# Kernel optimization log

Hardware: AMD Instinct MI355X
Metric: run time of the kernel (lower is better)

Reference implementation:

```python
import jax, jax.numpy as jnp
import numpy as np

D = 1024        # hidden_size
H = 16          # num_heads
HD = D // H     # head_dim = 64
K = 4           # conv kernel size
I = int(D * 2.7)  # ffn intermediate = 2764
B, T = 2, 2048
EPS = 1e-6
GATE_BIAS = 4.0


def setup_inputs() -> dict:
    key = jax.random.key(0)
    ks = jax.random.split(key, 16)
    s = D ** -0.5
    return {
        "x": jax.random.normal(ks[0], (B, T, D), jnp.float32),
        "norm1_w": jnp.ones((D,), jnp.float32),
        "norm2_w": jnp.ones((D,), jnp.float32),
        "conv_w": jax.random.normal(ks[1], (D, K), jnp.float32) * 0.2,
        "conv_b": jnp.zeros((D,), jnp.float32),
        "wq": jax.random.normal(ks[2], (D, D), jnp.float32) * s,
        "wk": jax.random.normal(ks[3], (D, D), jnp.float32) * s,
        "wv": jax.random.normal(ks[4], (D, D), jnp.float32) * s,
        "wb": jax.random.normal(ks[5], (D, H), jnp.float32) * s,
        "wa": jax.random.normal(ks[6], (D, H), jnp.float32) * s,
        "wo": jax.random.normal(ks[7], (D, D), jnp.float32) * s,
        "wg": jax.random.normal(ks[8], (D, I), jnp.float32) * s,
        "wu": jax.random.normal(ks[9], (D, I), jnp.float32) * s,
        "wd": jax.random.normal(ks[10], (I, D), jnp.float32) * (I ** -0.5),
    }


def _rmsnorm(x, w):
    return x * jax.lax.rsqrt(jnp.mean(x * x, axis=-1, keepdims=True) + EPS) * w


def _causal_depthwise_conv(x, conv_w, conv_b):
    # x: [B,T,D]; depthwise causal conv, kernel K, then SiLU
    xt = jnp.transpose(x, (0, 2, 1))  # [B,D,T]
    y = jax.lax.conv_general_dilated(
        xt, conv_w[:, None, :],  # [D,1,K]
        window_strides=(1,), padding=[(K - 1, 0)],
        feature_group_count=D,
        dimension_numbers=("NCH", "OIH", "NCH"))
    y = jnp.transpose(y, (0, 2, 1)) + conv_b  # [B,T,D]
    return jax.nn.silu(y)


def _l2norm(x):
    return x * jax.lax.rsqrt(jnp.sum(x * x, axis=-1, keepdims=True) + EPS)


def _gated_delta_rule(xc, wq, wk, wv, wb, wa):
    b, t = xc.shape[0], xc.shape[1]
    q = _l2norm((xc @ wq).reshape(b, t, H, HD))
    k = _l2norm((xc @ wk).reshape(b, t, H, HD))
    v = (xc @ wv).reshape(b, t, H, HD)
    beta = jax.nn.sigmoid(xc @ wb)              # [B,T,H]
    alpha = jax.nn.sigmoid(xc @ wa + GATE_BIAS)  # [B,T,H] decay gate

    # time-major for scan
    qt = jnp.moveaxis(q, 1, 0)
    kt = jnp.moveaxis(k, 1, 0)
    vt = jnp.moveaxis(v, 1, 0)
    bt = jnp.moveaxis(beta, 1, 0)
    at = jnp.moveaxis(alpha, 1, 0)

    S0 = jnp.zeros((b, H, HD, HD), xc.dtype)  # [B,H,dk,dv]

    def step(S, inp):
        q_, k_, v_, b_, a_ = inp
        S = a_[..., None, None] * S
        pred = jnp.einsum("bhkv,bhk->bhv", S, k_)
        S = S + k_[..., :, None] * (b_[..., None] * (v_ - pred))[..., None, :]
        o = jnp.einsum("bhkv,bhk->bhv", S, q_)
        return S, o

    _, o = jax.lax.scan(step, S0, (qt, kt, vt, bt, at))  # [T,B,H,HD]
    return jnp.moveaxis(o, 1, 0).reshape(b, t, D)


def reference(x, norm1_w, norm2_w, conv_w, conv_b, wq, wk, wv, wb, wa, wo,
              wg, wu, wd):
    residual = x
    xn = _rmsnorm(x, norm1_w)
    xc = _causal_depthwise_conv(xn, conv_w, conv_b)
    mixer_out = _gated_delta_rule(xc, wq, wk, wv, wb, wa) @ wo
    h = residual + mixer_out
    hn = _rmsnorm(h, norm2_w)
    ffn = (jax.nn.silu(hn @ wg) * (hn @ wu)) @ wd
    return h + ffn
```

## Files before the change

kernel.cpp:

```cpp
#include <hip/hip_runtime.h>
#include <math.h>

#define D_ 1024
#define H_ 16
#define HD_ 64
#define KW_ 4
#define I_ 2764
#define IP_ 2816
#define NQKV_ 3328
#define NGU_ 5632
#define B_ 2
#define T_ 2048
#define BT_ (B_*T_)
#define ND_ (BT_*D_)
#define NH_ (BT_*H_)
#define NCH_ 32
#define NG_ (32*NCH_)
#define EPS_ 1e-6f
#define GATE_BIAS_ 4.0f

typedef __attribute__((ext_vector_type(8))) short bf16x8;
typedef __attribute__((ext_vector_type(4))) float f32x4;

#define MFMA_(a,b,c) __builtin_amdgcn_mfma_f32_16x16x32_bf16(a, b, c, 0, 0, 0)
#define GLDS_(src, dst) __builtin_amdgcn_global_load_lds( \
    (const __attribute__((address_space(1))) void*)(src), \
    (__attribute__((address_space(3))) void*)(dst), 16, 0, 0)

__device__ float f_sc1[BT_];
__device__ float f_be[NH_];
__device__ float f_al[NH_];
__device__ float f_h[ND_];
__device__ float g_rs[NG_ * 256];
__device__ float g_BmT[(size_t)NG_*4096];
__device__ unsigned short g_Gqk[(size_t)NG_*4096];
__device__ unsigned short g_Y[(size_t)NG_*4096];
__device__ unsigned short g_ZT[(size_t)NG_*4096];
__device__ unsigned short g_A[(size_t)NG_*4096];
__device__ unsigned short g_S[(size_t)NG_*4096];
__device__ unsigned short b_q[ND_];
__device__ unsigned short b_k[ND_];
__device__ unsigned short b_v[ND_];
__device__ unsigned short b_xc[ND_];
__device__ unsigned short b_o[ND_];
__device__ unsigned short b_hn[ND_];
__device__ unsigned short b_f[(size_t)BT_*IP_];
__device__ unsigned short b_wqkvT[(size_t)NQKV_*D_];
__device__ unsigned short b_woT[D_*D_];
__device__ unsigned short b_wguT[(size_t)NGU_*D_];
__device__ unsigned short b_wdT[(size_t)D_*IP_];

__device__ __forceinline__ unsigned short f2b(float x) {
  union { float f; unsigned u; } a; a.f = x;
  unsigned r = a.u + 0x7fff + ((a.u >> 16) & 1);
  return (unsigned short)(r >> 16);
}
__device__ __forceinline__ float b2f(unsigned short s) {
  union { unsigned u; float f; } a; a.u = ((unsigned)s) << 16; return a.f;
}

__device__ __forceinline__ const unsigned short* bsel(int id) {
  switch (id) {
    case 0: return b_xc;  case 1: return b_o;    case 2: return b_hn;
    case 3: return b_f;   case 4: return b_wqkvT; case 5: return b_woT;
    case 6: return b_wguT; default: return b_wdT;
  }
}
__device__ __forceinline__ unsigned short* bselw(int id) {
  return (unsigned short*)bsel(id);
}

__global__ __launch_bounds__(256) void rmssc_k(const float* __restrict__ x) {
  int row = blockIdx.x;
  int tid = threadIdx.x;
  float4 v = ((const float4*)(x + (size_t)row * D_))[tid];
  float ss = v.x*v.x + v.y*v.y + v.z*v.z + v.w*v.w;
  #pragma unroll
  for (int o = 32; o > 0; o >>= 1) ss += __shfl_down(ss, o);
  __shared__ float sred[4];
  if ((tid & 63) == 0) sred[tid >> 6] = ss;
  __syncthreads();
  if (tid == 0)
    f_sc1[row] = rsqrtf((sred[0]+sred[1]+sred[2]+sred[3]) / (float)D_ + EPS_);
}

__global__ __launch_bounds__(256) void rms2_k(const float* __restrict__ w) {
  int row = blockIdx.x;
  const float* xr = f_h + (size_t)row * D_;
  int tid = threadIdx.x;
  float4 v = ((const float4*)xr)[tid];
  float ss = v.x*v.x + v.y*v.y + v.z*v.z + v.w*v.w;
  #pragma unroll
  for (int o = 32; o > 0; o >>= 1) ss += __shfl_down(ss, o);
  __shared__ float sred[4];
  __shared__ float sscale;
  if ((tid & 63) == 0) sred[tid >> 6] = ss;
  __syncthreads();
  if (tid == 0)
    sscale = rsqrtf((sred[0]+sred[1]+sred[2]+sred[3]) / (float)D_ + EPS_);
  __syncthreads();
  float s = sscale;
  float4 wv = ((const float4*)w)[tid];
  unsigned short* orow = b_hn + (size_t)row * D_ + tid * 4;
  orow[0] = f2b(v.x*s*wv.x); orow[1] = f2b(v.y*s*wv.y);
  orow[2] = f2b(v.z*s*wv.z); orow[3] = f2b(v.w*s*wv.w);
}

__global__ __launch_bounds__(256) void conv2_k(const float* __restrict__ x,
                                               const float* __restrict__ cw,
                                               const float* __restrict__ cb,
                                               const float* __restrict__ n1w) {
  int idx = blockIdx.x * 256 + threadIdx.x;
  int d = idx & (D_ - 1);
  int bt = idx >> 10;
  int t = bt & (T_ - 1);
  float wd = n1w[d];
  float acc = cb[d];
  #pragma unroll
  for (int j = 0; j < KW_; j++) {
    int tt = t - (KW_ - 1) + j;
    if (tt >= 0) {
      int off = j - (KW_ - 1);
      acc += x[(size_t)idx + (size_t)off * D_] * f_sc1[bt + off] * wd * cw[d * KW_ + j];
    }
  }
  float s = acc / (1.f + expf(-acc));
  b_xc[idx] = f2b(s);
}

__global__ __launch_bounds__(256) void castTqkv_k(const float* __restrict__ wq,
                                                  const float* __restrict__ wk,
                                                  const float* __restrict__ wv,
                                                  const float* __restrict__ wb,
                                                  const float* __restrict__ wa) {
  __shared__ float s[64][65];
  int n0 = blockIdx.x * 64, k0 = blockIdx.y * 64;
  int tx = threadIdx.x & 63, ty = threadIdx.x >> 6;
  int nn = n0 + tx;
  const float* src = nullptr; int col = 0, ld = 1024;
  if (nn < 1024)      { src = wq; col = nn; }
  else if (nn < 2048) { src = wk; col = nn - 1024; }
  else if (nn < 3072) { src = wv; col = nn - 2048; }
  else if (nn < 3088) { src = wb; col = nn - 3072; ld = 16; }
  else if (nn < 3104) { src = wa; col = nn - 3088; ld = 16; }
  #pragma unroll
  for (int j = ty; j < 64; j += 4)
    s[j][tx] = src ? src[(size_t)(k0 + j) * ld + col] : 0.f;
  __syncthreads();
  #pragma unroll
  for (int j = ty; j < 64; j += 4)
    b_wqkvT[(size_t)(n0 + j) * D_ + k0 + tx] = f2b(s[tx][j]);
}

__global__ __launch_bounds__(256) void castTgu_k(const float* __restrict__ wg,
                                                 const float* __restrict__ wu) {
  __shared__ float s[64][65];
  int n0 = blockIdx.x * 64, k0 = blockIdx.y * 64;
  int tx = threadIdx.x & 63, ty = threadIdx.x >> 6;
  int nn = n0 + tx;
  int inner = nn & 31;
  int col = (nn >> 5) * 16 + (inner & 15);
  const float* src = (inner < 16) ? wg : wu;
  bool ok = (col < I_);
  #pragma unroll
  for (int j = ty; j < 64; j += 4)
    s[j][tx] = ok ? src[(size_t)(k0 + j) * I_ + col] : 0.f;
  __syncthreads();
  #pragma unroll
  for (int j = ty; j < 64; j += 4)
    b_wguT[(size_t)(n0 + j) * D_ + k0 + tx] = f2b(s[tx][j]);
}

__global__ __launch_bounds__(256) void castT_k(const float* __restrict__ W,
                                               int K, int N, int outid, int Kp) {
  __shared__ float s[64][65];
  unsigned short* out = bselw(outid);
  int k0 = blockIdx.y * 64, n0 = blockIdx.x * 64;
  int tx = threadIdx.x & 63, ty = threadIdx.x >> 6;
  #pragma unroll
  for (int j = ty; j < 64; j += 4) {
    int kk = k0 + j, nn = n0 + tx;
    s[j][tx] = (kk < K && nn < N) ? W[(size_t)kk * N + nn] : 0.f;
  }
  __syncthreads();
  #pragma unroll
  for (int j = ty; j < 64; j += 4)
    out[(size_t)(n0 + j) * Kp + k0 + tx] = f2b(s[tx][j]);
}

__global__ __launch_bounds__(512) void gemm256(int aid, int bid, int Kp, int mode) {
  __shared__ __align__(16) unsigned short Al[2][256 * 64];
  __shared__ __align__(16) unsigned short Bl[2][256 * 64];
  const unsigned short* A = bsel(aid);
  const unsigned short* Bt = bsel(bid);
  int tid = threadIdx.x;
  int nbx = gridDim.x;
  int nwg = nbx * gridDim.y;
  int lid = blockIdx.y * nbx + blockIdx.x;
  int cpx = nwg >> 3;
  int swzb = (lid & 7) * cpx + (lid >> 3);
  int m0 = (swzb / nbx) * 256, n0 = (swzb % nbx) * 256;
  int w = tid >> 6, lane = tid & 63;
  int wm = (w >> 2) * 128, wn = (w & 3) * 64;
  const int l15 = lane & 15, lg = lane >> 4;
  int srow = tid >> 3;
  int scol = ((tid & 7) ^ (srow & 7)) * 8;
  int ldsw = w * 512;
  const unsigned short* Arow = A + (size_t)m0 * Kp;
  const unsigned short* Brow = Bt + (size_t)n0 * Kp;
  int swz0 = ((0 + lg) ^ (l15 & 7)) * 8;
  int swz1 = ((4 + lg) ^ (l15 & 7)) * 8;
  f32x4 acc[8][4] = {};
  const int nt = Kp >> 6;
  #pragma unroll
  for (int i = 0; i < 4; i++) {
    GLDS_(Arow + (size_t)(i * 64 + srow) * Kp + scol, Al[0] + i * 4096 + ldsw);
    GLDS_(Brow + (size_t)(i * 64 + srow) * Kp + scol, Bl[0] + i * 4096 + ldsw);
  }
  asm volatile("s_waitcnt vmcnt(0)" ::: "memory");
  __builtin_amdgcn_s_barrier();
  int cur = 0;
  for (int t = 0; t < nt; t++) {
    if (t + 1 < nt) {
      int k0 = (t + 1) << 6;
      #pragma unroll
      for (int i = 0; i < 4; i++) {
        GLDS_(Arow + (size_t)(i * 64 + srow) * Kp + k0 + scol, Al[cur ^ 1] + i * 4096 + ldsw);
        GLDS_(Brow + (size_t)(i * 64 + srow) * Kp + k0 + scol, Bl[cur ^ 1] + i * 4096 + ldsw);
      }
    }
    __builtin_amdgcn_s_setprio(1);
    {
      bf16x8 af[8], bf[4];
      #pragma unroll
      for (int i = 0; i < 8; i++)
        af[i] = *(const bf16x8*)&Al[cur][(wm + i * 16 + l15) * 64 + swz0];
      #pragma unroll
      for (int j = 0; j < 4; j++)
        bf[j] = *(const bf16x8*)&Bl[cur][(wn + j * 16 + l15) * 64 + swz0];
      #pragma unroll
      for (int i = 0; i < 8; i++)
        #pragma unroll
        for (int j = 0; j < 4; j++)
          acc[i][j] = MFMA_(af[i], bf[j], acc[i][j]);
      #pragma unroll
      for (int i = 0; i < 8; i++)
        af[i] = *(const bf16x8*)&Al[cur][(wm + i * 16 + l15) * 64 + swz1];
      #pragma unroll
      for (int j = 0; j < 4; j++)
        bf[j] = *(const bf16x8*)&Bl[cur][(wn + j * 16 + l15) * 64 + swz1];
      #pragma unroll
      for (int i = 0; i < 8; i++)
        #pragma unroll
        for (int j = 0; j < 4; j++)
          acc[i][j] = MFMA_(af[i], bf[j], acc[i][j]);
    }
    __builtin_amdgcn_s_setprio(0);
    __builtin_amdgcn_sched_barrier(0);
    asm volatile("s_waitcnt vmcnt(0)" ::: "memory");
    __builtin_amdgcn_s_barrier();
    __builtin_amdgcn_sched_barrier(0);
    cur ^= 1;
  }
  int C0 = n0 + wn;
  if (mode == 0) {
    if (C0 < 2048) {
      unsigned short* dst = (C0 < 1024) ? b_q : b_k;
      int cbase = C0 & 1023;
      #pragma unroll
      for (int i = 0; i < 8; i++) {
        int r0i = m0 + wm + i * 16 + lg * 4;
        #pragma unroll
        for (int r = 0; r < 4; r++) {
          float ss = acc[i][0][r]*acc[i][0][r] + acc[i][1][r]*acc[i][1][r]
                   + acc[i][2][r]*acc[i][2][r] + acc[i][3][r]*acc[i][3][r];
          ss += __shfl_xor(ss, 1); ss += __shfl_xor(ss, 2);
          ss += __shfl_xor(ss, 4); ss += __shfl_xor(ss, 8);
          float sc = rsqrtf(ss + EPS_);
          #pragma unroll
          for (int j = 0; j < 4; j++)
            dst[(size_t)(r0i + r) * D_ + cbase + j * 16 + l15] = f2b(acc[i][j][r] * sc);
        }
      }
    } else if (C0 < 3072) {
      int cbase = C0 & 1023;
      #pragma unroll
      for (int i = 0; i < 8; i++) {
        int r0i = m0 + wm + i * 16 + lg * 4;
        #pragma unroll
        for (int j = 0; j < 4; j++)
          #pragma unroll
          for (int r = 0; r < 4; r++)
            b_v[(size_t)(r0i + r) * D_ + cbase + j * 16 + l15] = f2b(acc[i][j][r]);
      }
    } else if (C0 == 3072) {
      #pragma unroll
      for (int i = 0; i < 8; i++) {
        int r0i = m0 + wm + i * 16 + lg * 4;
        #pragma unroll
        for (int r = 0; r < 4; r++) {
          float vb = acc[i][0][r];
          f_be[(size_t)(r0i + r) * H_ + l15] = 1.f / (1.f + expf(-vb));
          float va = acc[i][1][r] + GATE_BIAS_;
          f_al[(size_t)(r0i + r) * H_ + l15] = 1.f / (1.f + expf(-va));
        }
      }
    }
  } else {
    #pragma unroll
    for (int i = 0; i < 8; i++) {
      int r0i = m0 + wm + i * 16 + lg * 4;
      #pragma unroll
      for (int jp = 0; jp < 2; jp++) {
        int j = jp * 2;
        int Lbase = ((C0 + j * 16) >> 5) * 16;
        #pragma unroll
        for (int r = 0; r < 4; r++) {
          float g = acc[i][j][r], u = acc[i][j + 1][r];
          float sg = g / (1.f + expf(-g));
          b_f[(size_t)(r0i + r) * IP_ + Lbase + l15] = f2b(sg * u);
        }
      }
    }
  }
}

__global__ __launch_bounds__(256) void gemm_bf16(int aid, int bid, int Kp, int mode,
                                                 const float* __restrict__ ext,
                                                 float* __restrict__ eout) {
  __shared__ __align__(16) unsigned short Al[3][128 * 32];
  __shared__ __align__(16) unsigned short Bl[3][128 * 32];
  const unsigned short* A = bsel(aid);
  const unsigned short* Bt = bsel(bid);
  int tid = threadIdx.x;
  int nbx = gridDim.x;
  int nwg = nbx * gridDim.y;
  int lid = blockIdx.y * nbx + blockIdx.x;
  int cpx = nwg >> 3;
  int swzb = (lid & 7) * cpx + (lid >> 3);
  int m0 = (swzb / nbx) * 128, n0 = (swzb % nbx) * 128;
  int wave = tid >> 6, lane = tid & 63;
  int wm = (wave >> 1) * 64, wn = (wave & 1) * 64;
  int lrow = tid >> 2;
  int lcol = ((tid & 3) ^ ((lrow >> 1) & 3)) * 8;
  f32x4 acc[4][4] = {};
  const int l15 = lane & 15, lg = lane >> 4;
  const int sw = (lg ^ ((l15 >> 1) & 3)) * 8;
  const int nt = Kp >> 5;
  const unsigned short* Arow = A + (size_t)m0 * Kp;
  const unsigned short* Brow = Bt + (size_t)n0 * Kp;
  {
    GLDS_(Arow + (size_t)lrow * Kp + lcol,        Al[0] + wave * 512);
    GLDS_(Arow + (size_t)(64 + lrow) * Kp + lcol, Al[0] + 2048 + wave * 512);
    GLDS_(Brow + (size_t)lrow * Kp + lcol,        Bl[0] + wave * 512);
    GLDS_(Brow + (size_t)(64 + lrow) * Kp + lcol, Bl[0] + 2048 + wave * 512);
    GLDS_(Arow + (size_t)lrow * Kp + 32 + lcol,        Al[1] + wave * 512);
    GLDS_(Arow + (size_t)(64 + lrow) * Kp + 32 + lcol, Al[1] + 2048 + wave * 512);
    GLDS_(Brow + (size_t)lrow * Kp + 32 + lcol,        Bl[1] + wave * 512);
    GLDS_(Brow + (size_t)(64 + lrow) * Kp + 32 + lcol, Bl[1] + 2048 + wave * 512);
  }
  int c0i = 0, c1i = 1, c2i = 2;
  for (int t = 0; t < nt; t++) {
    if (t + 2 < nt) {
      int k0 = (t + 2) << 5;
      GLDS_(Arow + (size_t)lrow * Kp + k0 + lcol,        Al[c2i] + wave * 512);
      GLDS_(Arow + (size_t)(64 + lrow) * Kp + k0 + lcol, Al[c2i] + 2048 + wave * 512);
      GLDS_(Brow + (size_t)lrow * Kp + k0 + lcol,        Bl[c2i] + wave * 512);
      GLDS_(Brow + (size_t)(64 + lrow) * Kp + k0 + lcol, Bl[c2i] + 2048 + wave * 512);
      asm volatile("s_waitcnt vmcnt(8)" ::: "memory");
    } else if (t + 1 < nt) {
      asm volatile("s_waitcnt vmcnt(4)" ::: "memory");
    } else {
      asm volatile("s_waitcnt vmcnt(0)" ::: "memory");
    }
    __builtin_amdgcn_sched_barrier(0);
    __builtin_amdgcn_s_barrier();
    __builtin_amdgcn_sched_barrier(0);
    bf16x8 af[4], bf[4];
    #pragma unroll
    for (int i = 0; i < 4; i++)
      af[i] = *(const bf16x8*)&Al[c0i][(wm + i * 16 + l15) * 32 + sw];
    #pragma unroll
    for (int j = 0; j < 4; j++)
      bf[j] = *(const bf16x8*)&Bl[c0i][(wn + j * 16 + l15) * 32 + sw];
    #pragma unroll
    for (int i = 0; i < 4; i++)
      #pragma unroll
      for (int j = 0; j < 4; j++)
        acc[i][j] = MFMA_(af[i], bf[j], acc[i][j]);
    __builtin_amdgcn_sched_barrier(0);
    __builtin_amdgcn_s_barrier();
    __builtin_amdgcn_sched_barrier(0);
    int tmp = c0i; c0i = c1i; c1i = c2i; c2i = tmp;
  }
  int C0 = n0 + wn;
  if (mode == 2) {
    #pragma unroll
    for (int i = 0; i < 4; i++) {
      int r0i = m0 + wm + i * 16 + lg * 4;
      #pragma unroll
      for (int j = 0; j < 4; j++)
        #pragma unroll
        for (int r = 0; r < 4; r++) {
          size_t off = (size_t)(r0i + r) * D_ + C0 + j * 16 + l15;
          f_h[off] = ext[off] + acc[i][j][r];
        }
    }
  } else {
    #pragma unroll
    for (int i = 0; i < 4; i++) {
      int r0i = m0 + wm + i * 16 + lg * 4;
      #pragma unroll
      for (int j = 0; j < 4; j++)
        #pragma unroll
        for (int r = 0; r < 4; r++) {
          size_t off = (size_t)(r0i + r) * D_ + C0 + j * 16 + l15;
          eout[off] = f_h[off] + acc[i][j][r];
        }
    }
  }
}


__global__ __launch_bounds__(256) void prep_k() {
  __shared__ __align__(16) char sm[40448];
  unsigned short* sKT = (unsigned short*)sm;
  unsigned short* sVT = (unsigned short*)(sm + 10240);
  unsigned short* sAb = (unsigned short*)(sm + 20480);
  unsigned short* sYT = (unsigned short*)(sm + 20480);
  unsigned short* sXb = (unsigned short*)(sm + 29696);
  float* sL  = (float*)(sm + 38912);
  float* sB  = (float*)(sm + 39168);
  float* sS2 = (float*)(sm + 39424);
  float* sDec= (float*)(sm + 39680);
  float* sGC = (float*)(sm + 39936);

  int gid = blockIdx.x;
  int ch = gid & 31, bh = gid >> 5;
  int b = bh >> 4, h = bh & 15;
  int c0 = ch * 64, hb = h * HD_;
  int rowb = b * T_ + c0;
  int tid = threadIdx.x;
  int w = tid >> 6, lane = tid & 63, l15 = lane & 15, lg = lane >> 4;
  size_t g4 = (size_t)gid * 4096;

  if (tid < 64) {
    size_t rb = ((size_t)(rowb + tid)) * H_ + h;
    float la = log2f(f_al[rb]);
    #pragma unroll
    for (int m = 1; m < 64; m <<= 1) {
      float o = __shfl_up(la, m);
      if (tid >= m) la += o;
    }
    float L63 = __shfl(la, 63);
    float bt = f_be[rb];
    float g = exp2f(la);
    sL[tid] = la; sB[tid] = bt; sS2[tid] = bt * g;
    sDec[tid] = exp2f(L63 - la);
    if (tid == 63) sGC[0] = g;
    g_rs[(size_t)gid*256 + tid*4 + 0] = bt;
    g_rs[(size_t)gid*256 + tid*4 + 1] = bt * g;
    g_rs[(size_t)gid*256 + tid*4 + 2] = g;
  }
  __syncthreads();

  {
    int tp = tid >> 3, q8 = tid & 7;
    int t0 = 2 * tp, t1 = 2 * tp + 1;
    const bf16x8 k0 = *(const bf16x8*)(b_k + (size_t)(rowb + t0) * D_ + hb + q8 * 8);
    const bf16x8 k1 = *(const bf16x8*)(b_k + (size_t)(rowb + t1) * D_ + hb + q8 * 8);
    const bf16x8 v0 = *(const bf16x8*)(b_v + (size_t)(rowb + t0) * D_ + hb + q8 * 8);
    const bf16x8 v1 = *(const bf16x8*)(b_v + (size_t)(rowb + t1) * D_ + hb + q8 * 8);
    float s0 = sB[t0], s1v = sB[t1];
    unsigned* KT32 = (unsigned*)sKT;
    unsigned* VT32 = (unsigned*)sVT;
    #pragma unroll
    for (int i = 0; i < 8; i++) {
      int k = q8 * 8 + i;
      KT32[k*40 + tp] = (unsigned)(unsigned short)k0[i] |
                        ((unsigned)(unsigned short)k1[i] << 16);
      unsigned lo = f2b(b2f((unsigned short)v0[i]) * s0);
      unsigned hi = f2b(b2f((unsigned short)v1[i]) * s1v);
      VT32[k*40 + tp] = lo | (hi << 16);
    }
  }
  {
    bf16x8 bK[2], aK[4][2], aQ[4][2];
    #pragma unroll
    for (int k2 = 0; k2 < 2; k2++) {
      bK[k2] = *(const bf16x8*)&b_k[(size_t)(rowb + w*16 + l15)*D_ + hb + k2*32 + lg*8];
      #pragma unroll
      for (int ti = 0; ti < 4; ti++) {
        aK[ti][k2] = *(const bf16x8*)&b_k[(size_t)(rowb + ti*16 + l15)*D_ + hb + k2*32 + lg*8];
        aQ[ti][k2] = *(const bf16x8*)&b_q[(size_t)(rowb + ti*16 + l15)*D_ + hb + k2*32 + lg*8];
      }
    }
    f32x4 ck[4] = {}, cq[4] = {};
    #pragma unroll
    for (int k2 = 0; k2 < 2; k2++)
      #pragma unroll
      for (int ti = 0; ti < 4; ti++) {
        ck[ti] = MFMA_(aK[ti][k2], bK[k2], ck[ti]);
        cq[ti] = MFMA_(aQ[ti][k2], bK[k2], cq[ti]);
      }
    int j = w*16 + l15;
    float Lj = sL[j];
    #pragma unroll
    for (int ti = 0; ti < 4; ti++)
      #pragma unroll
      for (int r = 0; r < 4; r++) {
        int t = ti*16 + lg*4 + r;
        float ratio = exp2f(sL[t] - Lj);
        sAb[t*72 + j] = f2b((j < t) ? sB[t] * ratio * ck[ti][r] : 0.f);
        g_Gqk[g4 + t*64 + j] = f2b((j <= t) ? ratio * cq[ti][r] : 0.f);
      }
  }
  __syncthreads();
  {
    int c = (w << 4) + (lane >> 2);
    int p = lane & 3;
    int rb16 = p << 4;
    float xr[16];
    #pragma unroll
    for (int j = 0; j < 16; j++) xr[j] = 0.f;
    #pragma unroll
    for (int q = 0; q < 16; q++) {
      int r0 = 4 * q;
      const unsigned short* abr = sAb + r0 * 72 + rb16;
      bf16x8 A0a = *(const bf16x8*)(abr);
      bf16x8 A0b = *(const bf16x8*)(abr + 8);
      bf16x8 A1a = *(const bf16x8*)(abr + 72);
      bf16x8 A1b = *(const bf16x8*)(abr + 80);
      bf16x8 A2a = *(const bf16x8*)(abr + 144);
      bf16x8 A2b = *(const bf16x8*)(abr + 152);
      bf16x8 A3a = *(const bf16x8*)(abr + 216);
      bf16x8 A3b = *(const bf16x8*)(abr + 224);
      float s0 = 0.f, s1 = 0.f, s2 = 0.f, s3 = 0.f;
      #pragma unroll
      for (int j = 0; j < 8; j++) {
        float xv = xr[j], xw = xr[8 + j];
        s0 = fmaf(b2f((unsigned short)A0a[j]), xv, s0);
        s1 = fmaf(b2f((unsigned short)A1a[j]), xv, s1);
        s2 = fmaf(b2f((unsigned short)A2a[j]), xv, s2);
        s3 = fmaf(b2f((unsigned short)A3a[j]), xv, s3);
        s0 = fmaf(b2f((unsigned short)A0b[j]), xw, s0);
        s1 = fmaf(b2f((unsigned short)A1b[j]), xw, s1);
        s2 = fmaf(b2f((unsigned short)A2b[j]), xw, s2);
        s3 = fmaf(b2f((unsigned short)A3b[j]), xw, s3);
      }
      s0 += __shfl_xor(s0, 1); s0 += __shfl_xor(s0, 2);
      s1 += __shfl_xor(s1, 1); s1 += __shfl_xor(s1, 2);
      s2 += __shfl_xor(s2, 1); s2 += __shfl_xor(s2, 2);
      s3 += __shfl_xor(s3, 1); s3 += __shfl_xor(s3, 2);
      float a10 = b2f(sAb[(r0+1)*72 + r0]);
      float a20 = b2f(sAb[(r0+2)*72 + r0]);
      float a21 = b2f(sAb[(r0+2)*72 + r0+1]);
      float a30 = b2f(sAb[(r0+3)*72 + r0]);
      float a31 = b2f(sAb[(r0+3)*72 + r0+1]);
      float a32 = b2f(sAb[(r0+3)*72 + r0+2]);
      float x0 = ((r0+0) == c ? 1.f : 0.f) - s0;
      float x1 = ((r0+1) == c ? 1.f : 0.f) - s1 - a10*x0;
      float x2 = ((r0+2) == c ? 1.f : 0.f) - s2 - a20*x0 - a21*x1;
      float x3 = ((r0+3) == c ? 1.f : 0.f) - s3 - a30*x0 - a31*x1 - a32*x2;
      if (p == (q >> 2)) {
        int ji = 4 * (q & 3);
        xr[ji+0] = x0; xr[ji+1] = x1; xr[ji+2] = x2; xr[ji+3] = x3;
      }
    }
    #pragma unroll
    for (int j = 0; j < 16; j++)
      sXb[(rb16 + j)*72 + c] = f2b(xr[j]);
  }
  __syncthreads();
  int m0 = w * 16;
  f32x4 cyT[4], cz[4];
  {
    bf16x8 aKT[2];
    aKT[0] = *(const bf16x8*)&sKT[(m0 + l15)*80 + lg*8];
    aKT[1] = *(const bf16x8*)&sKT[(m0 + l15)*80 + 32 + lg*8];
    #pragma unroll
    for (int n = 0; n < 4; n++) {
      cyT[n] = f32x4{0.f, 0.f, 0.f, 0.f};
      #pragma unroll
      for (int k2 = 0; k2 < 2; k2++) {
        bf16x8 bb;
        #pragma unroll
        for (int i = 0; i < 8; i++) {
          int tp = k2*32 + lg*8 + i;
          bb[i] = (short)f2b(b2f(sXb[(n*16 + l15)*72 + tp]) * sS2[tp]);
        }
        cyT[n] = MFMA_(aKT[k2], bb, cyT[n]);
      }
    }
    bf16x8 aT2[2];
    #pragma unroll
    for (int k2 = 0; k2 < 2; k2++)
      #pragma unroll
      for (int i = 0; i < 8; i++) {
        int tp = k2*32 + lg*8 + i;
        aT2[k2][i] = (short)f2b(b2f(sXb[(m0 + l15)*72 + tp]) * sS2[tp]);
      }
    #pragma unroll
    for (int n = 0; n < 4; n++) {
      f32x4 c = {};
      #pragma unroll
      for (int k2 = 0; k2 < 2; k2++) {
        bf16x8 bKT = *(const bf16x8*)&sKT[(n*16 + l15)*80 + k2*32 + lg*8];
        c = MFMA_(aT2[k2], bKT, c);
      }
      #pragma unroll
      for (int r = 0; r < 4; r++)
        g_Y[g4 + (m0 + lg*4 + r)*64 + n*16 + l15] = f2b(c[r]);
    }
    bf16x8 aV[2];
    aV[0] = *(const bf16x8*)&sVT[(m0 + l15)*80 + lg*8];
    aV[1] = *(const bf16x8*)&sVT[(m0 + l15)*80 + 32 + lg*8];
    #pragma unroll
    for (int n = 0; n < 4; n++) {
      cz[n] = f32x4{0.f, 0.f, 0.f, 0.f};
      #pragma unroll
      for (int k2 = 0; k2 < 2; k2++) {
        bf16x8 bT = *(const bf16x8*)&sXb[(n*16 + l15)*72 + k2*32 + lg*8];
        cz[n] = MFMA_(aV[k2], bT, cz[n]);
      }
      #pragma unroll
      for (int r = 0; r < 4; r++)
        g_ZT[g4 + (m0 + lg*4 + r)*64 + n*16 + l15] = f2b(cz[n][r]);
    }
  }
  __syncthreads();
  #pragma unroll
  for (int n = 0; n < 4; n++)
    #pragma unroll
    for (int r = 0; r < 4; r++) {
      sYT[(m0 + lg*4 + r)*72 + n*16 + l15] = f2b(cyT[n][r]);
      sVT[(m0 + lg*4 + r)*80 + n*16 + l15] = f2b(cz[n][r]);
    }
  {
    int xx = tid >> 2, q = tid & 3;
    bf16x8 v0 = *(const bf16x8*)&sKT[xx*80 + q*16];
    bf16x8 v1 = *(const bf16x8*)&sKT[xx*80 + q*16 + 8];
    bf16x8 d0, d1;
    #pragma unroll
    for (int i = 0; i < 8; i++) {
      d0[i] = (short)f2b(b2f((unsigned short)v0[i]) * sDec[q*16 + i]);
      d1[i] = (short)f2b(b2f((unsigned short)v1[i]) * sDec[q*16 + 8 + i]);
    }
    *(bf16x8*)&sKT[xx*80 + q*16] = d0;
    *(bf16x8*)&sKT[xx*80 + q*16 + 8] = d1;
  }
  __syncthreads();
  {
    float gC = sGC[0];
    bf16x8 aKd[2];
    aKd[0] = *(const bf16x8*)&sKT[(m0 + l15)*80 + lg*8];
    aKd[1] = *(const bf16x8*)&sKT[(m0 + l15)*80 + 32 + lg*8];
    #pragma unroll
    for (int n = 0; n < 4; n++) {
      f32x4 c = {};
      #pragma unroll
      for (int k2 = 0; k2 < 2; k2++) {
        bf16x8 bY = *(const bf16x8*)&sYT[(n*16 + l15)*72 + k2*32 + lg*8];
        c = MFMA_(aKd[k2], bY, c);
      }
      #pragma unroll
      for (int r = 0; r < 4; r++) {
        int row = m0 + lg*4 + r, col = n*16 + l15;
        g_A[g4 + row*64 + col] = f2b(((row == col) ? gC : 0.f) - c[r]);
      }
    }
    #pragma unroll
    for (int n = 0; n < 4; n++) {
      f32x4 c = {};
      #pragma unroll
      for (int k2 = 0; k2 < 2; k2++) {
        bf16x8 bZ = *(const bf16x8*)&sVT[(n*16 + l15)*80 + k2*32 + lg*8];
        c = MFMA_(aKd[k2], bZ, c);
      }
      *(f32x4*)&g_BmT[g4 + (size_t)(n*16 + l15)*64 + m0 + lg*4] = c;
    }
  }
}

__global__ __launch_bounds__(256) void seq_k() {
  __shared__ __align__(16) unsigned short sST[4][16*80];
  int bh = blockIdx.x;
  int tid = threadIdx.x, w = tid >> 6, lane = tid & 63;
  int l15 = lane & 15, lg = lane >> 4;
  unsigned short* st = sST[w];
  for (int i = lane; i < 16*80; i += 64) st[i] = 0;
  f32x4 cerr[4] = {};
  bf16x8 aA[4][2];
  f32x4 cini[4];
  size_t g40 = (size_t)(bh * 32) * 4096;
  #pragma unroll
  for (int m = 0; m < 4; m++) {
    aA[m][0] = *(const bf16x8*)&g_A[g40 + (m*16 + l15)*64 + lg*8];
    aA[m][1] = *(const bf16x8*)&g_A[g40 + (m*16 + l15)*64 + 32 + lg*8];
    cini[m] = *(const f32x4*)&g_BmT[g40 + (w*16 + l15)*64 + m*16 + lg*4];
  }
  for (int ch = 0; ch < NCH_; ch++) {
    size_t gid = (size_t)bh * 32 + ch;
    float gC = g_rs[gid*256 + 254];
    bf16x8 bS0 = *(const bf16x8*)&st[l15*80 + lg*8];
    bf16x8 bS1 = *(const bf16x8*)&st[l15*80 + 32 + lg*8];
    *(bf16x8*)&g_S[gid*4096 + (w*16 + l15)*64 + lg*8] = bS0;
    *(bf16x8*)&g_S[gid*4096 + (w*16 + l15)*64 + 32 + lg*8] = bS1;
    bf16x8 aAn[4][2];
    f32x4 cin2[4];
    if (ch + 1 < NCH_) {
      size_t g4n = (gid + 1) * 4096;
      #pragma unroll
      for (int m = 0; m < 4; m++) {
        aAn[m][0] = *(const bf16x8*)&g_A[g4n + (m*16 + l15)*64 + lg*8];
        aAn[m][1] = *(const bf16x8*)&g_A[g4n + (m*16 + l15)*64 + 32 + lg*8];
        cin2[m] = *(const f32x4*)&g_BmT[g4n + (w*16 + l15)*64 + m*16 + lg*4];
      }
    }
    f32x4 c[4];
    #pragma unroll
    for (int m = 0; m < 4; m++) {
      #pragma unroll
      for (int r = 0; r < 4; r++)
        c[m][r] = cini[m][r] + gC * cerr[m][r];
      c[m] = MFMA_(aA[m][0], bS0, c[m]);
      c[m] = MFMA_(aA[m][1], bS1, c[m]);
    }
    #pragma unroll
    for (int m = 0; m < 4; m++)
      #pragma unroll
      for (int r = 0; r < 4; r++) {
        float x = c[m][r];
        unsigned short q = f2b(x);
        cerr[m][r] = x - b2f(q);
        st[l15*80 + m*16 + lg*4 + r] = q;
      }
    if (ch + 1 < NCH_) {
      #pragma unroll
      for (int m = 0; m < 4; m++) {
        aA[m][0] = aAn[m][0]; aA[m][1] = aAn[m][1];
        cini[m] = cin2[m];
      }
    }
  }
}

__global__ __launch_bounds__(256) void apply_k() {
  __shared__ __align__(16) unsigned short sUT[4][16*80];
  int gid = blockIdx.x;
  int ch = gid & 31, bh = gid >> 5;
  int b = bh >> 4, h = bh & 15;
  int c0 = ch * 64, hb = h * HD_;
  int rowb = b * T_ + c0;
  int tid = threadIdx.x, w = tid >> 6, lane = tid & 63;
  int l15 = lane & 15, lg = lane >> 4;
  unsigned short* ut = sUT[w];
  size_t g4 = (size_t)gid * 4096;
  bf16x8 aS[2];
  aS[0] = *(const bf16x8*)&g_S[g4 + (w*16 + l15)*64 + lg*8];
  aS[1] = *(const bf16x8*)&g_S[g4 + (w*16 + l15)*64 + 32 + lg*8];
  f32x4 cu[4];
  #pragma unroll
  for (int n = 0; n < 4; n++) {
    cu[n] = f32x4{0.f, 0.f, 0.f, 0.f};
    #pragma unroll
    for (int k2 = 0; k2 < 2; k2++) {
      bf16x8 bY = *(const bf16x8*)&g_Y[g4 + (n*16 + l15)*64 + k2*32 + lg*8];
      cu[n] = MFMA_(aS[k2], bY, cu[n]);
    }
  }
  #pragma unroll
  for (int n = 0; n < 4; n++)
    #pragma unroll
    for (int r = 0; r < 4; r++) {
      float zt = b2f(g_ZT[g4 + (w*16 + lg*4 + r)*64 + n*16 + l15]);
      ut[(lg*4 + r)*80 + n*16 + l15] = f2b(zt - cu[n][r]);
    }
  bf16x8 aU[2];
  aU[0] = *(const bf16x8*)&ut[l15*80 + lg*8];
  aU[1] = *(const bf16x8*)&ut[l15*80 + 32 + lg*8];
  f32x4 co[4];
  #pragma unroll
  for (int n = 0; n < 4; n++) {
    co[n] = f32x4{0.f, 0.f, 0.f, 0.f};
    #pragma unroll
    for (int k2 = 0; k2 < 2; k2++) {
      bf16x8 bQ = *(const bf16x8*)&b_q[(size_t)(rowb + n*16 + l15)*D_ + hb + k2*32 + lg*8];
      co[n] = MFMA_(aS[k2], bQ, co[n]);
    }
    float gm = g_rs[(size_t)gid*256 + (n*16 + l15)*4 + 2];
    #pragma unroll
    for (int r = 0; r < 4; r++) co[n][r] *= gm;
    #pragma unroll
    for (int k2 = 0; k2 < 2; k2++) {
      bf16x8 bG = *(const bf16x8*)&g_Gqk[g4 + (n*16 + l15)*64 + k2*32 + lg*8];
      co[n] = MFMA_(aU[k2], bG, co[n]);
    }
    ushort4 pk;
    pk.x = f2b(co[n][0]); pk.y = f2b(co[n][1]);
    pk.z = f2b(co[n][2]); pk.w = f2b(co[n][3]);
    *(ushort4*)&b_o[(size_t)(rowb + n*16 + l15)*D_ + hb + w*16 + lg*4] = pk;
  }
}

extern "C" void kernel_launch(void* const* d_in, const int* in_sizes, int n_in,
                              void* d_out, int out_size, void* d_ws, size_t ws_size,
                              hipStream_t stream) {
  const float* x   = (const float*)d_in[0];
  const float* n1w = (const float*)d_in[1];
  const float* n2w = (const float*)d_in[2];
  const float* cw  = (const float*)d_in[3];
  const float* cb  = (const float*)d_in[4];
  const float* wq  = (const float*)d_in[5];
  const float* wk  = (const float*)d_in[6];
  const float* wv  = (const float*)d_in[7];
  const float* wb  = (const float*)d_in[8];
  const float* wa  = (const float*)d_in[9];
  const float* wo  = (const float*)d_in[10];
  const float* wg  = (const float*)d_in[11];
  const float* wu  = (const float*)d_in[12];
  const float* wd  = (const float*)d_in[13];
  float* out = (float*)d_out;

  castTqkv_k<<<dim3(52, 16), 256, 0, stream>>>(wq, wk, wv, wb, wa);
  castT_k<<<dim3(16, 16), 256, 0, stream>>>(wo, D_, D_, 5, D_);
  castTgu_k<<<dim3(88, 16), 256, 0, stream>>>(wg, wu);
  castT_k<<<dim3(16, 44), 256, 0, stream>>>(wd, I_, D_, 7, IP_);

  rmssc_k<<<BT_, 256, 0, stream>>>(x);
  conv2_k<<<ND_ / 256, 256, 0, stream>>>(x, cw, cb, n1w);

  gemm256<<<dim3(13, 16), 512, 0, stream>>>(0, 4, D_, 0);

  prep_k<<<NG_, 256, 0, stream>>>();
  seq_k<<<32, 256, 0, stream>>>();
  apply_k<<<NG_, 256, 0, stream>>>();

  gemm_bf16<<<dim3(8, 32), 256, 0, stream>>>(1, 5, D_, 2, x, nullptr);
  rms2_k<<<BT_, 256, 0, stream>>>(n2w);
  gemm256<<<dim3(22, 16), 512, 0, stream>>>(2, 6, D_, 1);
  gemm_bf16<<<dim3(8, 32), 256, 0, stream>>>(3, 7, IP_, 3, nullptr, out);
}
```

Before: 433.9 us.

## Interleave GEMM main loop into four phases with staged global-to-LDS prefetch

Restructures the 256x256 bf16 GEMM K-loop into four sub-phases. Each phase loads two A row-fragments from LDS, issues a quarter of the next tile's global-to-LDS copies, synchronizes, then runs 16 MFMAs. The B fragments are loaded once per tile. This spreads memory traffic across the compute and overlaps it with MFMA work, in the style of ping-pong scheduling. The cost is four barrier pairs per tile instead of one, plus extra live registers for B.

```diff
diff --git a/kernel.cpp b/kernel.cpp
--- a/kernel.cpp
+++ b/kernel.cpp
@@ -219,48 +219,79 @@
   }
   asm volatile("s_waitcnt vmcnt(0)" ::: "memory");
   __builtin_amdgcn_s_barrier();
-  int cur = 0;
   for (int t = 0; t < nt; t++) {
-    if (t + 1 < nt) {
-      int k0 = (t + 1) << 6;
-      #pragma unroll
-      for (int i = 0; i < 4; i++) {
-        GLDS_(Arow + (size_t)(i * 64 + srow) * Kp + k0 + scol, Al[cur ^ 1] + i * 4096 + ldsw);
-        GLDS_(Brow + (size_t)(i * 64 + srow) * Kp + k0 + scol, Bl[cur ^ 1] + i * 4096 + ldsw);
-      }
-    }
-    __builtin_amdgcn_s_setprio(1);
+    int cur = t & 1;
+    int k0n = (t + 1) << 6;
+    bool more = (t + 1 < nt);
+    bf16x8 bf0[4], bf1[4];
     {
-      bf16x8 af[8], bf[4];
-      #pragma unroll
-      for (int i = 0; i < 8; i++)
-        af[i] = *(const bf16x8*)&Al[cur][(wm + i * 16 + l15) * 64 + swz0];
-      #pragma unroll
-      for (int j = 0; j < 4; j++)
-        bf[j] = *(const bf16x8*)&Bl[cur][(wn + j * 16 + l15) * 64 + swz0];
-      #pragma unroll
-      for (int i = 0; i < 8; i++)
-        #pragma unroll
-        for (int j = 0; j < 4; j++)
-          acc[i][j] = MFMA_(af[i], bf[j], acc[i][j]);
-      #pragma unroll
-      for (int i = 0; i < 8; i++)
-        af[i] = *(const bf16x8*)&Al[cur][(wm + i * 16 + l15) * 64 + swz1];
-      #pragma unroll
-      for (int j = 0; j < 4; j++)
-        bf[j] = *(const bf16x8*)&Bl[cur][(wn + j * 16 + l15) * 64 + swz1];
-      #pragma unroll
-      for (int i = 0; i < 8; i++)
-        #pragma unroll
-        for (int j = 0; j < 4; j++)
-          acc[i][j] = MFMA_(af[i], bf[j], acc[i][j]);
-    }
-    __builtin_amdgcn_s_setprio(0);
-    __builtin_amdgcn_sched_barrier(0);
-    asm volatile("s_waitcnt vmcnt(0)" ::: "memory");
-    __builtin_amdgcn_s_barrier();
-    __builtin_amdgcn_sched_barrier(0);
-    cur ^= 1;
+      #pragma unroll
+      for (int j = 0; j < 4; j++) {
+        bf0[j] = *(const bf16x8*)&Bl[cur][(wn + j * 16 + l15) * 64 + swz0];
+        bf1[j] = *(const bf16x8*)&Bl[cur][(wn + j * 16 + l15) * 64 + swz1];
+      }
+      bf16x8 a0k0 = *(const bf16x8*)&Al[cur][(wm + 0 * 16 + l15) * 64 + swz0];
+      bf16x8 a0k1 = *(const bf16x8*)&Al[cur][(wm + 0 * 16 + l15) * 64 + swz1];
+      bf16x8 a1k0 = *(const bf16x8*)&Al[cur][(wm + 1 * 16 + l15) * 64 + swz0];
+      bf16x8 a1k1 = *(const bf16x8*)&Al[cur][(wm + 1 * 16 + l15) * 64 + swz1];
+      if (more) {
+        GLDS_(Arow + (size_t)(0 * 64 + srow) * Kp + k0n + scol, Al[cur ^ 1] + 0 * 4096 + ldsw);
+        GLDS_(Arow + (size_t)(1 * 64 + srow) * Kp + k0n + scol, Al[cur ^ 1] + 1 * 4096 + ldsw);
+      }
+      __builtin_amdgcn_sched_barrier(0);
+      __builtin_amdgcn_s_barrier();
+      asm volatile("s_waitcnt lgkmcnt(0)" ::: "memory");
+      __builtin_amdgcn_sched_barrier(0);
+      __builtin_amdgcn_s_setprio(1);
+      #pragma unroll
+      for (int j = 0; j < 4; j++) {
+        acc[0][j] = MFMA_(a0k0, bf0[j], acc[0][j]);
+        acc[0][j] = MFMA_(a0k1, bf1[j], acc[0][j]);
+        acc[1][j] = MFMA_(a1k0, bf0[j], acc[1][j]);
+        acc[1][j] = MFMA_(a1k1, bf1[j], acc[1][j]);
+      }
+      __builtin_amdgcn_s_setprio(0);
+      __builtin_amdgcn_sched_barrier(0);
+      __builtin_amdgcn_s_barrier();
+      __builtin_amdgcn_sched_barrier(0);
+    }
+    #pragma unroll
+    for (int p = 1; p < 4; p++) {
+      bf16x8 a0k0 = *(const bf16x8*)&Al[cur][(wm + (2 * p) * 16 + l15) * 64 + swz0];
+      bf16x8 a0k1 = *(const bf16x8*)&Al[cur][(wm + (2 * p) * 16 + l15) * 64 + swz1];
+      bf16x8 a1k0 = *(const bf16x8*)&Al[cur][(wm + (2 * p + 1) * 16 + l15) * 64 + swz0];
+      bf16x8 a1k1 = *(const bf16x8*)&Al[cur][(wm + (2 * p + 1) * 16 + l15) * 64 + swz1];
+      if (more) {
+        if (p == 1) {
+          GLDS_(Arow + (size_t)(2 * 64 + srow) * Kp + k0n + scol, Al[cur ^ 1] + 2 * 4096 + ldsw);
+          GLDS_(Arow + (size_t)(3 * 64 + srow) * Kp + k0n + scol, Al[cur ^ 1] + 3 * 4096 + ldsw);
+        } else if (p == 2) {
+          GLDS_(Brow + (size_t)(0 * 64 + srow) * Kp + k0n + scol, Bl[cur ^ 1] + 0 * 4096 + ldsw);
+          GLDS_(Brow + (size_t)(1 * 64 + srow) * Kp + k0n + scol, Bl[cur ^ 1] + 1 * 4096 + ldsw);
+        } else {
+          GLDS_(Brow + (size_t)(2 * 64 + srow) * Kp + k0n + scol, Bl[cur ^ 1] + 2 * 4096 + ldsw);
+          GLDS_(Brow + (size_t)(3 * 64 + srow) * Kp + k0n + scol, Bl[cur ^ 1] + 3 * 4096 + ldsw);
+        }
+      }
+      __builtin_amdgcn_sched_barrier(0);
+      __builtin_amdgcn_s_barrier();
+      asm volatile("s_waitcnt lgkmcnt(0)" ::: "memory");
+      __builtin_amdgcn_sched_barrier(0);
+      __builtin_amdgcn_s_setprio(1);
+      #pragma unroll
+      for (int j = 0; j < 4; j++) {
+        acc[2 * p][j]     = MFMA_(a0k0, bf0[j], acc[2 * p][j]);
+        acc[2 * p][j]     = MFMA_(a0k1, bf1[j], acc[2 * p][j]);
+        acc[2 * p + 1][j] = MFMA_(a1k0, bf0[j], acc[2 * p + 1][j]);
+        acc[2 * p + 1][j] = MFMA_(a1k1, bf1[j], acc[2 * p + 1][j]);
+      }
+      __builtin_amdgcn_s_setprio(0);
+      __builtin_amdgcn_sched_barrier(0);
+      if (p == 3 && more)
+        asm volatile("s_waitcnt vmcnt(0)" ::: "memory");
+      __builtin_amdgcn_s_barrier();
+      __builtin_amdgcn_sched_barrier(0);
+    }
   }
   int C0 = n0 + wn;
   if (mode == 0) {
```

Result: faster. 420.5 us (-3.1%).
